# Kernel tuning notes

Hardware: AMD Instinct MI355X
Metric: run time of the kernel (lower is better)

The kernel has to match this reference:

```python
import jax, jax.numpy as jnp
import numpy as np

B, S, D, H = 2, 2048, 1024, 16
RANK = int(D * 0.2)  # 204, per decom(): rank = int(min(a,b)*ratio_LR)
HEAD = D // H


def setup_inputs() -> dict:
    key = jax.random.key(0)
    ks = jax.random.split(key, 16)
    s_in = 1.0 / np.sqrt(D)
    s_r = 1.0 / np.sqrt(RANK)
    inp = {
        'q': jax.random.normal(ks[0], (B, S, D), jnp.float32),
        'k': jax.random.normal(ks[1], (B, S, D), jnp.float32),
        'v': jax.random.normal(ks[2], (B, S, D), jnp.float32),
    }
    names = ['q', 'k', 'v', 'o']
    for i, n in enumerate(names):
        inp[f'V{n}'] = jax.random.uniform(ks[3 + 3 * i], (RANK, D), jnp.float32, -s_in, s_in)
        inp[f'U{n}'] = jax.random.uniform(ks[4 + 3 * i], (D, RANK), jnp.float32, -s_r, s_r)
        inp[f'b{n}'] = jax.random.uniform(ks[5 + 3 * i], (D,), jnp.float32, -s_r, s_r)
    return inp


def _factorized(x, Vw, Uw, b):
    # x @ V^T @ U^T + b  (low-rank linear: Linear(D->rank, no bias) then Linear(rank->D, bias))
    return jnp.einsum('bsr,dr->bsd', jnp.einsum('bsd,rd->bsr', x, Vw), Uw) + b


def _split_heads(x):
    # [B,S,D] -> [B,H,S,HEAD]
    return x.reshape(B, S, H, HEAD).transpose(0, 2, 1, 3)


def reference(q, k, v, Vq, Uq, bq, Vk, Uk, bk, Vv, Uv, bv, Vo, Uo, bo):
    qh = _split_heads(_factorized(q, Vq, Uq, bq))
    kh = _split_heads(_factorized(k, Vk, Uk, bk))
    vh = _split_heads(_factorized(v, Vv, Uv, bv))
    temperature = jnp.asarray(HEAD, jnp.float32) ** 0.5
    scores = jnp.einsum('bhqd,bhkd->bhqk', qh, kh) / temperature
    causal = jnp.tril(jnp.ones((S, S), bool))  # recreated each call in original
    scores = jnp.where(causal, scores, -jnp.inf)
    attn = jax.nn.softmax(scores, axis=-1)  # [B,H,S,S]
    out = jnp.einsum('bhqk,bhkd->bhqd', attn, vh)
    out = out.transpose(0, 2, 1, 3).reshape(B, S, D)
    out = _factorized(out, Vo, Uo, bo)
    # original returns attn flattened over batch*heads
    return out, attn.reshape(B * H, S, S)
```

## Files before the change

kernel.cpp:

```cpp
#include <hip/hip_runtime.h>
#include <stdint.h>

#define BB   2
#define SS   2048
#define DD   1024
#define NH   16
#define RK   204
#define RKP  256
#define HDIM 64
#define BH   (BB*NH)

typedef __attribute__((ext_vector_type(8))) short short8;
typedef __attribute__((ext_vector_type(4))) float f32x4;
typedef unsigned short u16;
typedef unsigned int   u32;

static __device__ __forceinline__ u16 f2bf(float f) {
    union { float f; u32 u; } v; v.f = f;
    u32 u = v.u;
    return (u16)((u + 0x7fffu + ((u >> 16) & 1u)) >> 16);
}
static __device__ __forceinline__ u32 pack2(float lo, float hi) {
    return (u32)f2bf(lo) | ((u32)f2bf(hi) << 16);
}

__global__ void cvt_bf16_k(const float* __restrict__ in, u16* __restrict__ out, int n4) {
    int i = blockIdx.x * blockDim.x + threadIdx.x;
    if (i < n4) {
        float4 f = ((const float4*)in)[i];
        u32 lo = pack2(f.x, f.y), hi = pack2(f.z, f.w);
        ((uint2*)out)[i] = make_uint2(lo, hi);
    }
}

__global__ void cvt_pad_u_k(const float* __restrict__ in, u16* __restrict__ out) {
    int i = blockIdx.x * blockDim.x + threadIdx.x;
    if (i >= DD * RKP) return;
    int row = i >> 8, col = i & (RKP - 1);
    out[i] = (col < RK) ? f2bf(in[row * RK + col]) : (u16)0;
}

__global__ void transpose_v_k(const u16* __restrict__ vh, u16* __restrict__ vT) {
    int i = blockIdx.x * blockDim.x + threadIdx.x;
    int s  = i & (SS - 1);
    int j  = i >> 11;
    int hd = j & (HDIM - 1);
    int bh = j >> 6;
    int b_ = bh >> 4, h = bh & (NH - 1);
    vT[i] = vh[(size_t)(b_*SS + s)*DD + h*HDIM + hd];
}

template<int A_F32, int OUT_F32, int HAS_BIAS>
__global__ __launch_bounds__(256)
void gemm_nt_k(const void* __restrict__ Ap, int lda,
               const u16* __restrict__ Bp, int ldb, int nrowsB,
               const float* __restrict__ bias,
               void* __restrict__ Cp, int ldc, int K)
{
    __shared__ __align__(16) u16 As[64*72];
    __shared__ __align__(16) u16 Bs[64*72];
    const int row0 = blockIdx.x * 64;
    const int col0 = blockIdx.y * 64;
    const int t = threadIdx.x;
    const int w = t >> 6, lane = t & 63, quad = lane >> 4, l16 = lane & 15;
    const int r = t >> 2, seg = t & 3;

    f32x4 acc0 = 0.f, acc1 = 0.f, acc2 = 0.f, acc3 = 0.f;

    for (int k0 = 0; k0 < K; k0 += 64) {
        __syncthreads();
        if (A_F32) {
            const float* ga = (const float*)Ap + (size_t)(row0 + r) * lda + k0 + seg*16;
            float4 f0 = ((const float4*)ga)[0];
            float4 f1 = ((const float4*)ga)[1];
            float4 f2 = ((const float4*)ga)[2];
            float4 f3 = ((const float4*)ga)[3];
            uint4 s0 = { pack2(f0.x,f0.y), pack2(f0.z,f0.w), pack2(f1.x,f1.y), pack2(f1.z,f1.w) };
            uint4 s1 = { pack2(f2.x,f2.y), pack2(f2.z,f2.w), pack2(f3.x,f3.y), pack2(f3.z,f3.w) };
            *(uint4*)(As + r*72 + seg*16)     = s0;
            *(uint4*)(As + r*72 + seg*16 + 8) = s1;
        } else {
            const u16* ga = (const u16*)Ap + (size_t)(row0 + r) * lda + k0 + seg*16;
            *(uint4*)(As + r*72 + seg*16)     = ((const uint4*)ga)[0];
            *(uint4*)(As + r*72 + seg*16 + 8) = ((const uint4*)ga)[1];
        }
        {
            uint4 b0 = {0,0,0,0}, b1 = {0,0,0,0};
            if (col0 + r < nrowsB) {
                const u16* gb = Bp + (size_t)(col0 + r) * ldb + k0 + seg*16;
                b0 = ((const uint4*)gb)[0];
                b1 = ((const uint4*)gb)[1];
            }
            *(uint4*)(Bs + r*72 + seg*16)     = b0;
            *(uint4*)(Bs + r*72 + seg*16 + 8) = b1;
        }
        __syncthreads();
        #pragma unroll
        for (int c = 0; c < 2; ++c) {
            short8 a = *(const short8*)(As + (w*16 + l16)*72 + c*32 + quad*8);
            short8 b0v = *(const short8*)(Bs + (0*16 + l16)*72 + c*32 + quad*8);
            acc0 = __builtin_amdgcn_mfma_f32_16x16x32_bf16(a, b0v, acc0, 0, 0, 0);
            short8 b1v = *(const short8*)(Bs + (1*16 + l16)*72 + c*32 + quad*8);
            acc1 = __builtin_amdgcn_mfma_f32_16x16x32_bf16(a, b1v, acc1, 0, 0, 0);
            short8 b2v = *(const short8*)(Bs + (2*16 + l16)*72 + c*32 + quad*8);
            acc2 = __builtin_amdgcn_mfma_f32_16x16x32_bf16(a, b2v, acc2, 0, 0, 0);
            short8 b3v = *(const short8*)(Bs + (3*16 + l16)*72 + c*32 + quad*8);
            acc3 = __builtin_amdgcn_mfma_f32_16x16x32_bf16(a, b3v, acc3, 0, 0, 0);
        }
    }

    #pragma unroll
    for (int f = 0; f < 4; ++f) {
        f32x4 a = (f==0) ? acc0 : (f==1) ? acc1 : (f==2) ? acc2 : acc3;
        int col = col0 + f*16 + l16;
        float bv = HAS_BIAS ? bias[col] : 0.f;
        #pragma unroll
        for (int rg = 0; rg < 4; ++rg) {
            int rowg = row0 + w*16 + quad*4 + rg;
            float val = a[rg] + bv;
            if (col >= nrowsB) val = 0.f;
            if (OUT_F32) ((float*)Cp)[(size_t)rowg*ldc + col] = val;
            else         ((u16*)Cp)[(size_t)rowg*ldc + col]  = f2bf(val);
        }
    }
}

__global__ __launch_bounds__(256)
void attn_ml_k(const u16* __restrict__ qh, const u16* __restrict__ kh,
               float* __restrict__ mbuf, float* __restrict__ lbuf)
{
    __shared__ __align__(16) u16 Ks[64*72];
    const int blk = blockIdx.x;
    const int qt = blk & 31, bh = blk >> 5;
    const int b_ = bh >> 4, h = bh & (NH - 1);
    const int qbase = qt * 64;
    const int t = threadIdx.x, w = t >> 6, lane = t & 63, quad = lane >> 4, l16 = lane & 15;
    const int r = t >> 2, seg = t & 3;
    const float scl = 0.125f;

    const u16* qrow = qh + (size_t)(b_*SS + qbase + w*16 + l16)*DD + h*HDIM;
    short8 q0 = *(const short8*)(qrow + quad*8);
    short8 q1 = *(const short8*)(qrow + 32 + quad*8);

    float m[4], l[4];
    #pragma unroll
    for (int rg = 0; rg < 4; ++rg) { m[rg] = -INFINITY; l[rg] = 0.f; }

    for (int kt = 0; kt <= qt; ++kt) {
        int kbase = kt * 64;
        __syncthreads();
        const u16* krow = kh + (size_t)(b_*SS + kbase + r)*DD + h*HDIM + seg*16;
        uint4 kv0 = ((const uint4*)krow)[0];
        uint4 kv1 = ((const uint4*)krow)[1];
        *(uint4*)(Ks + r*72 + seg*16)     = kv0;
        *(uint4*)(Ks + r*72 + seg*16 + 8) = kv1;
        __syncthreads();

        f32x4 sa0 = 0.f, sa1 = 0.f, sa2 = 0.f, sa3 = 0.f;
        {
            short8 b0 = *(const short8*)(Ks + (0*16 + l16)*72 + quad*8);
            sa0 = __builtin_amdgcn_mfma_f32_16x16x32_bf16(q0, b0, sa0, 0,0,0);
            short8 b0b = *(const short8*)(Ks + (0*16 + l16)*72 + 32 + quad*8);
            sa0 = __builtin_amdgcn_mfma_f32_16x16x32_bf16(q1, b0b, sa0, 0,0,0);
            short8 b1 = *(const short8*)(Ks + (1*16 + l16)*72 + quad*8);
            sa1 = __builtin_amdgcn_mfma_f32_16x16x32_bf16(q0, b1, sa1, 0,0,0);
            short8 b1b = *(const short8*)(Ks + (1*16 + l16)*72 + 32 + quad*8);
            sa1 = __builtin_amdgcn_mfma_f32_16x16x32_bf16(q1, b1b, sa1, 0,0,0);
            short8 b2 = *(const short8*)(Ks + (2*16 + l16)*72 + quad*8);
            sa2 = __builtin_amdgcn_mfma_f32_16x16x32_bf16(q0, b2, sa2, 0,0,0);
            short8 b2b = *(const short8*)(Ks + (2*16 + l16)*72 + 32 + quad*8);
            sa2 = __builtin_amdgcn_mfma_f32_16x16x32_bf16(q1, b2b, sa2, 0,0,0);
            short8 b3 = *(const short8*)(Ks + (3*16 + l16)*72 + quad*8);
            sa3 = __builtin_amdgcn_mfma_f32_16x16x32_bf16(q0, b3, sa3, 0,0,0);
            short8 b3b = *(const short8*)(Ks + (3*16 + l16)*72 + 32 + quad*8);
            sa3 = __builtin_amdgcn_mfma_f32_16x16x32_bf16(q1, b3b, sa3, 0,0,0);
        }
        int key0 = kbase + l16;
        #pragma unroll
        for (int rg = 0; rg < 4; ++rg) {
            int qg = qbase + w*16 + quad*4 + rg;
            float v0 = (key0      <= qg) ? sa0[rg]*scl : -INFINITY;
            float v1 = (key0 + 16 <= qg) ? sa1[rg]*scl : -INFINITY;
            float v2 = (key0 + 32 <= qg) ? sa2[rg]*scl : -INFINITY;
            float v3 = (key0 + 48 <= qg) ? sa3[rg]*scl : -INFINITY;
            float mx = fmaxf(fmaxf(v0, v1), fmaxf(v2, v3));
            #pragma unroll
            for (int d = 1; d < 16; d <<= 1) mx = fmaxf(mx, __shfl_xor(mx, d));
            float nm = fmaxf(m[rg], mx);
            float ssum = __expf(v0 - nm) + __expf(v1 - nm) + __expf(v2 - nm) + __expf(v3 - nm);
            #pragma unroll
            for (int d = 1; d < 16; d <<= 1) ssum += __shfl_xor(ssum, d);
            l[rg] = l[rg] * __expf(m[rg] - nm) + ssum;
            m[rg] = nm;
        }
    }
    if (l16 == 0) {
        #pragma unroll
        for (int rg = 0; rg < 4; ++rg) {
            int qg = qbase + w*16 + quad*4 + rg;
            mbuf[bh*SS + qg] = m[rg];
            lbuf[bh*SS + qg] = l[rg];
        }
    }
}

__global__ __launch_bounds__(256)
void attn_av_k(const u16* __restrict__ qh, const u16* __restrict__ kh,
               const u16* __restrict__ vT,
               const float* __restrict__ mbuf, const float* __restrict__ lbuf,
               float* __restrict__ attn_out, u16* __restrict__ Ob)
{
    __shared__ __align__(16) u16 Ks[64*72];
    __shared__ __align__(16) u16 Vs[64*72];
    __shared__ __align__(16) u16 Ps[64*72];
    const int blk = blockIdx.x;
    const int qt = blk & 31, bh = blk >> 5;
    const int b_ = bh >> 4, h = bh & (NH - 1);
    const int qbase = qt * 64;
    const int t = threadIdx.x, w = t >> 6, lane = t & 63, quad = lane >> 4, l16 = lane & 15;
    const int r = t >> 2, seg = t & 3;
    const float scl = 0.125f;

    const u16* qrow = qh + (size_t)(b_*SS + qbase + w*16 + l16)*DD + h*HDIM;
    short8 q0 = *(const short8*)(qrow + quad*8);
    short8 q1 = *(const short8*)(qrow + 32 + quad*8);

    float mr[4], rl[4];
    #pragma unroll
    for (int rg = 0; rg < 4; ++rg) {
        int qg = qbase + w*16 + quad*4 + rg;
        mr[rg] = mbuf[bh*SS + qg];
        rl[rg] = 1.f / lbuf[bh*SS + qg];
    }
    f32x4 oa0 = 0.f, oa1 = 0.f, oa2 = 0.f, oa3 = 0.f;
    float* attn_base = attn_out + (size_t)bh * SS * SS;

    for (int kt = 0; kt < 32; ++kt) {
        int kbase = kt * 64;
        if (kbase > qbase + 63) {
            float4 z = {0.f, 0.f, 0.f, 0.f};
            float* p = attn_base + (size_t)(qbase + r)*SS + kbase + seg*16;
            ((float4*)p)[0] = z; ((float4*)p)[1] = z; ((float4*)p)[2] = z; ((float4*)p)[3] = z;
            continue;
        }
        __syncthreads();
        {
            const u16* krow = kh + (size_t)(b_*SS + kbase + r)*DD + h*HDIM + seg*16;
            *(uint4*)(Ks + r*72 + seg*16)     = ((const uint4*)krow)[0];
            *(uint4*)(Ks + r*72 + seg*16 + 8) = ((const uint4*)krow)[1];
            const u16* vrow = vT + ((size_t)(bh*HDIM + r))*SS + kbase + seg*16;
            *(uint4*)(Vs + r*72 + seg*16)     = ((const uint4*)vrow)[0];
            *(uint4*)(Vs + r*72 + seg*16 + 8) = ((const uint4*)vrow)[1];
        }
        __syncthreads();

        f32x4 sa0 = 0.f, sa1 = 0.f, sa2 = 0.f, sa3 = 0.f;
        {
            short8 b0 = *(const short8*)(Ks + (0*16 + l16)*72 + quad*8);
            sa0 = __builtin_amdgcn_mfma_f32_16x16x32_bf16(q0, b0, sa0, 0,0,0);
            short8 b0b = *(const short8*)(Ks + (0*16 + l16)*72 + 32 + quad*8);
            sa0 = __builtin_amdgcn_mfma_f32_16x16x32_bf16(q1, b0b, sa0, 0,0,0);
            short8 b1 = *(const short8*)(Ks + (1*16 + l16)*72 + quad*8);
            sa1 = __builtin_amdgcn_mfma_f32_16x16x32_bf16(q0, b1, sa1, 0,0,0);
            short8 b1b = *(const short8*)(Ks + (1*16 + l16)*72 + 32 + quad*8);
            sa1 = __builtin_amdgcn_mfma_f32_16x16x32_bf16(q1, b1b, sa1, 0,0,0);
            short8 b2 = *(const short8*)(Ks + (2*16 + l16)*72 + quad*8);
            sa2 = __builtin_amdgcn_mfma_f32_16x16x32_bf16(q0, b2, sa2, 0,0,0);
            short8 b2b = *(const short8*)(Ks + (2*16 + l16)*72 + 32 + quad*8);
            sa2 = __builtin_amdgcn_mfma_f32_16x16x32_bf16(q1, b2b, sa2, 0,0,0);
            short8 b3 = *(const short8*)(Ks + (3*16 + l16)*72 + quad*8);
            sa3 = __builtin_amdgcn_mfma_f32_16x16x32_bf16(q0, b3, sa3, 0,0,0);
            short8 b3b = *(const short8*)(Ks + (3*16 + l16)*72 + 32 + quad*8);
            sa3 = __builtin_amdgcn_mfma_f32_16x16x32_bf16(q1, b3b, sa3, 0,0,0);
        }

        #pragma unroll
        for (int f = 0; f < 4; ++f) {
            f32x4 sv = (f==0) ? sa0 : (f==1) ? sa1 : (f==2) ? sa2 : sa3;
            int key = kbase + f*16 + l16;
            #pragma unroll
            for (int rg = 0; rg < 4; ++rg) {
                int qg = qbase + w*16 + quad*4 + rg;
                float p = (key <= qg) ? __expf(sv[rg]*scl - mr[rg]) * rl[rg] : 0.f;
                attn_base[(size_t)qg*SS + key] = p;
                Ps[(w*16 + quad*4 + rg)*72 + f*16 + l16] = f2bf(p);
            }
        }
        __syncthreads();

        #pragma unroll
        for (int c = 0; c < 2; ++c) {
            short8 pa = *(const short8*)(Ps + (w*16 + l16)*72 + c*32 + quad*8);
            short8 v0 = *(const short8*)(Vs + (0*16 + l16)*72 + c*32 + quad*8);
            oa0 = __builtin_amdgcn_mfma_f32_16x16x32_bf16(pa, v0, oa0, 0,0,0);
            short8 v1 = *(const short8*)(Vs + (1*16 + l16)*72 + c*32 + quad*8);
            oa1 = __builtin_amdgcn_mfma_f32_16x16x32_bf16(pa, v1, oa1, 0,0,0);
            short8 v2 = *(const short8*)(Vs + (2*16 + l16)*72 + c*32 + quad*8);
            oa2 = __builtin_amdgcn_mfma_f32_16x16x32_bf16(pa, v2, oa2, 0,0,0);
            short8 v3 = *(const short8*)(Vs + (3*16 + l16)*72 + c*32 + quad*8);
            oa3 = __builtin_amdgcn_mfma_f32_16x16x32_bf16(pa, v3, oa3, 0,0,0);
        }
    }

    #pragma unroll
    for (int f = 0; f < 4; ++f) {
        f32x4 ov = (f==0) ? oa0 : (f==1) ? oa1 : (f==2) ? oa2 : oa3;
        #pragma unroll
        for (int rg = 0; rg < 4; ++rg) {
            int qg = qbase + w*16 + quad*4 + rg;
            Ob[(size_t)(b_*SS + qg)*DD + h*HDIM + f*16 + l16] = f2bf(ov[rg]);
        }
    }
}

extern "C" void kernel_launch(void* const* d_in, const int* in_sizes, int n_in,
                              void* d_out, int out_size, void* d_ws, size_t ws_size,
                              hipStream_t stream)
{
    const float* xs[3] = { (const float*)d_in[0], (const float*)d_in[1], (const float*)d_in[2] };
    const float* Vw[4] = { (const float*)d_in[3], (const float*)d_in[6], (const float*)d_in[9],  (const float*)d_in[12] };
    const float* Uw[4] = { (const float*)d_in[4], (const float*)d_in[7], (const float*)d_in[10], (const float*)d_in[13] };
    const float* bw[4] = { (const float*)d_in[5], (const float*)d_in[8], (const float*)d_in[11], (const float*)d_in[14] };

    char* ws = (char*)d_ws;
    size_t off = 0;
    auto alloc = [&](size_t bytes) -> char* {
        char* p = ws + off;
        off += (bytes + 255) & ~(size_t)255;
        return p;
    };
    u16* wV[4]; for (int i = 0; i < 4; ++i) wV[i] = (u16*)alloc((size_t)RK*DD*2);
    u16* wU[4]; for (int i = 0; i < 4; ++i) wU[i] = (u16*)alloc((size_t)DD*RKP*2);
    u16* Tb  = (u16*)alloc((size_t)BB*SS*RKP*2);
    u16* hb[3]; for (int i = 0; i < 3; ++i) hb[i] = (u16*)alloc((size_t)BB*SS*DD*2);
    u16* vTb = (u16*)alloc((size_t)BB*SS*DD*2);
    float* mbuf = (float*)alloc((size_t)BH*SS*4);
    float* lbuf = (float*)alloc((size_t)BH*SS*4);
    u16* Ob  = (u16*)alloc((size_t)BB*SS*DD*2);
    (void)ws_size; (void)in_sizes; (void)n_in; (void)out_size;

    for (int i = 0; i < 4; ++i)
        cvt_bf16_k<<<(RK*DD/4 + 255)/256, 256, 0, stream>>>(Vw[i], wV[i], RK*DD/4);
    for (int i = 0; i < 4; ++i)
        cvt_pad_u_k<<<(DD*RKP + 255)/256, 256, 0, stream>>>(Uw[i], wU[i]);

    const int MROWS = BB*SS;
    for (int p = 0; p < 3; ++p) {
        gemm_nt_k<1,0,0><<<dim3(MROWS/64, RKP/64), 256, 0, stream>>>(
            xs[p], DD, wV[p], DD, RK, nullptr, Tb, RKP, DD);
        gemm_nt_k<0,0,1><<<dim3(MROWS/64, DD/64), 256, 0, stream>>>(
            Tb, RKP, wU[p], RKP, DD, bw[p], hb[p], DD, RKP);
    }
    transpose_v_k<<<(BB*SS*DD)/256, 256, 0, stream>>>(hb[2], vTb);

    float* attn_out = (float*)d_out + (size_t)BB*SS*DD;
    attn_ml_k<<<BH*32, 256, 0, stream>>>(hb[0], hb[1], mbuf, lbuf);
    attn_av_k<<<BH*32, 256, 0, stream>>>(hb[0], hb[1], vTb, mbuf, lbuf, attn_out, Ob);

    gemm_nt_k<0,0,0><<<dim3(MROWS/64, RKP/64), 256, 0, stream>>>(
        Ob, DD, wV[3], DD, RK, nullptr, Tb, RKP, DD);
    gemm_nt_k<0,1,1><<<dim3(MROWS/64, DD/64), 256, 0, stream>>>(
        Tb, RKP, wU[3], RKP, DD, bw[3], d_out, DD, RKP);
}
```

Before: 888.8 us.

## Defer softmax stat reductions, specialize diagonal masking, tile the V transpose

The row max/sum pass now keeps per-lane online-softmax statistics and merges them across the 16 lanes with a single shuffle reduction after the key loop, instead of shuffling twice per tile. Masking is applied only on the diagonal tile, and off-diagonal tiles take a mask-free path in both attention kernels. The block-wide barrier after the P tile is written to LDS becomes a compiler-only fence, which relies on each wave reading back only its own rows of that tile. The V transpose becomes an LDS-tiled kernel with 16-byte loads and stores, and the zero-fill of the masked-out region moves to a separate loop after the compute loop; -INFINITY is replaced by a large negative sentinel.

```diff
diff --git a/kernel.cpp b/kernel.cpp
--- a/kernel.cpp
+++ b/kernel.cpp
@@ -15,6 +15,8 @@
 typedef unsigned short u16;
 typedef unsigned int   u32;
 
+#define NEGBIG (-1e30f)
+
 static __device__ __forceinline__ u16 f2bf(float f) {
     union { float f; u32 u; } v; v.f = f;
     u32 u = v.u;
@@ -40,14 +42,26 @@
     out[i] = (col < RK) ? f2bf(in[row * RK + col]) : (u16)0;
 }
 
-__global__ void transpose_v_k(const u16* __restrict__ vh, u16* __restrict__ vT) {
-    int i = blockIdx.x * blockDim.x + threadIdx.x;
-    int s  = i & (SS - 1);
-    int j  = i >> 11;
-    int hd = j & (HDIM - 1);
-    int bh = j >> 6;
-    int b_ = bh >> 4, h = bh & (NH - 1);
-    vT[i] = vh[(size_t)(b_*SS + s)*DD + h*HDIM + hd];
+__global__ __launch_bounds__(256)
+void transpose_v_k(const u16* __restrict__ vh, u16* __restrict__ vT) {
+    __shared__ __align__(16) u16 T[64*72];
+    const int blk = blockIdx.x;
+    const int st = blk & 31, bh = blk >> 5;
+    const int b_ = bh >> 4, h = bh & (NH - 1);
+    const int t = threadIdx.x;
+    const int r = t >> 2, seg = t & 3;
+
+    const u16* src = vh + (size_t)(b_*SS + st*64 + r)*DD + h*HDIM + seg*16;
+    __align__(16) u16 vs_[16];
+    *(uint4*)(vs_ + 0) = ((const uint4*)src)[0];
+    *(uint4*)(vs_ + 8) = ((const uint4*)src)[1];
+    #pragma unroll
+    for (int j = 0; j < 16; ++j) T[(seg*16 + j)*72 + r] = vs_[j];
+    __syncthreads();
+
+    u16* dst = vT + ((size_t)bh*HDIM + r)*SS + st*64 + seg*16;
+    ((uint4*)dst)[0] = *(const uint4*)(T + r*72 + seg*16);
+    ((uint4*)dst)[1] = *(const uint4*)(T + r*72 + seg*16 + 8);
 }
 
 template<int A_F32, int OUT_F32, int HAS_BIAS>
@@ -144,7 +158,7 @@
 
     float m[4], l[4];
     #pragma unroll
-    for (int rg = 0; rg < 4; ++rg) { m[rg] = -INFINITY; l[rg] = 0.f; }
+    for (int rg = 0; rg < 4; ++rg) { m[rg] = NEGBIG; l[rg] = 0.f; }
 
     for (int kt = 0; kt <= qt; ++kt) {
         int kbase = kt * 64;
@@ -175,22 +189,49 @@
             short8 b3b = *(const short8*)(Ks + (3*16 + l16)*72 + 32 + quad*8);
             sa3 = __builtin_amdgcn_mfma_f32_16x16x32_bf16(q1, b3b, sa3, 0,0,0);
         }
-        int key0 = kbase + l16;
-        #pragma unroll
-        for (int rg = 0; rg < 4; ++rg) {
-            int qg = qbase + w*16 + quad*4 + rg;
-            float v0 = (key0      <= qg) ? sa0[rg]*scl : -INFINITY;
-            float v1 = (key0 + 16 <= qg) ? sa1[rg]*scl : -INFINITY;
-            float v2 = (key0 + 32 <= qg) ? sa2[rg]*scl : -INFINITY;
-            float v3 = (key0 + 48 <= qg) ? sa3[rg]*scl : -INFINITY;
-            float mx = fmaxf(fmaxf(v0, v1), fmaxf(v2, v3));
+
+        if (kt < qt) {
             #pragma unroll
-            for (int d = 1; d < 16; d <<= 1) mx = fmaxf(mx, __shfl_xor(mx, d));
-            float nm = fmaxf(m[rg], mx);
-            float ssum = __expf(v0 - nm) + __expf(v1 - nm) + __expf(v2 - nm) + __expf(v3 - nm);
+            for (int rg = 0; rg < 4; ++rg) {
+                float v0 = sa0[rg]*scl, v1 = sa1[rg]*scl, v2 = sa2[rg]*scl, v3 = sa3[rg]*scl;
+                float m4 = fmaxf(fmaxf(v0, v1), fmaxf(v2, v3));
+                float nm = fmaxf(m[rg], m4);
+                l[rg] = l[rg]*__expf(m[rg]-nm)
+                      + (__expf(v0-nm)+__expf(v1-nm)) + (__expf(v2-nm)+__expf(v3-nm));
+                m[rg] = nm;
+            }
+        } else {
+            int key0 = kbase + l16;
             #pragma unroll
-            for (int d = 1; d < 16; d <<= 1) ssum += __shfl_xor(ssum, d);
-            l[rg] = l[rg] * __expf(m[rg] - nm) + ssum;
+            for (int rg = 0; rg < 4; ++rg) {
+                int qg = qbase + w*16 + quad*4 + rg;
+                bool c0 = (key0      <= qg), c1 = (key0 + 16 <= qg);
+                bool c2 = (key0 + 32 <= qg), c3 = (key0 + 48 <= qg);
+                float v0 = c0 ? sa0[rg]*scl : NEGBIG;
+                float v1 = c1 ? sa1[rg]*scl : NEGBIG;
+                float v2 = c2 ? sa2[rg]*scl : NEGBIG;
+                float v3 = c3 ? sa3[rg]*scl : NEGBIG;
+                float m4 = fmaxf(fmaxf(v0, v1), fmaxf(v2, v3));
+                float nm = fmaxf(m[rg], m4);
+                float e0 = c0 ? __expf(v0-nm) : 0.f;
+                float e1 = c1 ? __expf(v1-nm) : 0.f;
+                float e2 = c2 ? __expf(v2-nm) : 0.f;
+                float e3 = c3 ? __expf(v3-nm) : 0.f;
+                float corr = (m[rg] > NEGBIG) ? __expf(m[rg]-nm) : 0.f;
+                l[rg] = l[rg]*corr + (e0+e1) + (e2+e3);
+                m[rg] = nm;
+            }
+        }
+    }
+
+    #pragma unroll
+    for (int rg = 0; rg < 4; ++rg) {
+        #pragma unroll
+        for (int d = 1; d < 16; d <<= 1) {
+            float mo = __shfl_xor(m[rg], d);
+            float lo = __shfl_xor(l[rg], d);
+            float nm = fmaxf(m[rg], mo);
+            l[rg] = l[rg]*__expf(m[rg]-nm) + lo*__expf(mo-nm);
             m[rg] = nm;
         }
     }
@@ -235,14 +276,8 @@
     f32x4 oa0 = 0.f, oa1 = 0.f, oa2 = 0.f, oa3 = 0.f;
     float* attn_base = attn_out + (size_t)bh * SS * SS;
 
-    for (int kt = 0; kt < 32; ++kt) {
+    for (int kt = 0; kt <= qt; ++kt) {
         int kbase = kt * 64;
-        if (kbase > qbase + 63) {
-            float4 z = {0.f, 0.f, 0.f, 0.f};
-            float* p = attn_base + (size_t)(qbase + r)*SS + kbase + seg*16;
-            ((float4*)p)[0] = z; ((float4*)p)[1] = z; ((float4*)p)[2] = z; ((float4*)p)[3] = z;
-            continue;
-        }
         __syncthreads();
         {
             const u16* krow = kh + (size_t)(b_*SS + kbase + r)*DD + h*HDIM + seg*16;
@@ -274,19 +309,34 @@
             sa3 = __builtin_amdgcn_mfma_f32_16x16x32_bf16(q1, b3b, sa3, 0,0,0);
         }
 
-        #pragma unroll
-        for (int f = 0; f < 4; ++f) {
-            f32x4 sv = (f==0) ? sa0 : (f==1) ? sa1 : (f==2) ? sa2 : sa3;
-            int key = kbase + f*16 + l16;
+        if (kt < qt) {
             #pragma unroll
-            for (int rg = 0; rg < 4; ++rg) {
-                int qg = qbase + w*16 + quad*4 + rg;
-                float p = (key <= qg) ? __expf(sv[rg]*scl - mr[rg]) * rl[rg] : 0.f;
-                attn_base[(size_t)qg*SS + key] = p;
-                Ps[(w*16 + quad*4 + rg)*72 + f*16 + l16] = f2bf(p);
+            for (int f = 0; f < 4; ++f) {
+                f32x4 sv = (f==0) ? sa0 : (f==1) ? sa1 : (f==2) ? sa2 : sa3;
+                int key = kbase + f*16 + l16;
+                #pragma unroll
+                for (int rg = 0; rg < 4; ++rg) {
+                    int qg = qbase + w*16 + quad*4 + rg;
+                    float p = __expf(sv[rg]*scl - mr[rg]) * rl[rg];
+                    attn_base[(size_t)qg*SS + key] = p;
+                    Ps[(w*16 + quad*4 + rg)*72 + f*16 + l16] = f2bf(p);
+                }
             }
-        }
-        __syncthreads();
+        } else {
+            #pragma unroll
+            for (int f = 0; f < 4; ++f) {
+                f32x4 sv = (f==0) ? sa0 : (f==1) ? sa1 : (f==2) ? sa2 : sa3;
+                int key = kbase + f*16 + l16;
+                #pragma unroll
+                for (int rg = 0; rg < 4; ++rg) {
+                    int qg = qbase + w*16 + quad*4 + rg;
+                    float p = (key <= qg) ? __expf(sv[rg]*scl - mr[rg]) * rl[rg] : 0.f;
+                    attn_base[(size_t)qg*SS + key] = p;
+                    Ps[(w*16 + quad*4 + rg)*72 + f*16 + l16] = f2bf(p);
+                }
+            }
+        }
+        asm volatile("" ::: "memory");
 
         #pragma unroll
         for (int c = 0; c < 2; ++c) {
@@ -300,6 +350,13 @@
             short8 v3 = *(const short8*)(Vs + (3*16 + l16)*72 + c*32 + quad*8);
             oa3 = __builtin_amdgcn_mfma_f32_16x16x32_bf16(pa, v3, oa3, 0,0,0);
         }
+    }
+
+    for (int kt = qt + 1; kt < 32; ++kt) {
+        int kbase = kt * 64;
+        float4 z = {0.f, 0.f, 0.f, 0.f};
+        float* p = attn_base + (size_t)(qbase + r)*SS + kbase + seg*16;
+        ((float4*)p)[0] = z; ((float4*)p)[1] = z; ((float4*)p)[2] = z; ((float4*)p)[3] = z;
     }
 
     #pragma unroll
@@ -351,7 +408,7 @@
         gemm_nt_k<0,0,1><<<dim3(MROWS/64, DD/64), 256, 0, stream>>>(
             Tb, RKP, wU[p], RKP, DD, bw[p], hb[p], DD, RKP);
     }
-    transpose_v_k<<<(BB*SS*DD)/256, 256, 0, stream>>>(hb[2], vTb);
+    transpose_v_k<<<BH*32, 256, 0, stream>>>(hb[2], vTb);
 
     float* attn_out = (float*)d_out + (size_t)BB*SS*DD;
     attn_ml_k<<<BH*32, 256, 0, stream>>>(hb[0], hb[1], mbuf, lbuf);
```

Result: faster. 837.1 us (-5.8%).
